# Kernel optimization log

Hardware: AMD Instinct MI355X
Metric: run time of the kernel (lower is better)

## Reference

```python
import jax, jax.numpy as jnp
import numpy as np

N_NODES = 50000
N_EDGES = 600000
N_GRAPHS = 256
IN_C = 128
HID = 128
OUT_C = 2


def setup_inputs() -> dict:
    key = jax.random.key(0)
    ks = jax.random.split(key, 16)
    d = {}
    d["x"] = jax.random.normal(ks[0], (N_NODES, IN_C), jnp.float32)
    d["edge_index"] = jax.random.randint(ks[1], (2, N_EDGES), 0, N_NODES, dtype=jnp.int32)
    d["root_node_idx"] = jax.random.randint(ks[2], (N_GRAPHS,), 0, N_NODES, dtype=jnp.int32)
    d["batch"] = jnp.sort(jax.random.randint(ks[3], (N_NODES,), 0, N_GRAPHS, dtype=jnp.int32))
    dims = [(IN_C, HID), (HID, HID), (HID, HID), (HID, HID)]
    for i, (ci, co) in enumerate(dims, start=1):
        s = 1.0 / np.sqrt(ci)
        d[f"w{i}_l"] = jax.random.uniform(ks[3 + i], (co, ci), jnp.float32, -s, s)
        d[f"b{i}_l"] = jnp.zeros((co,), jnp.float32)
        d[f"w{i}_r"] = jax.random.uniform(ks[7 + i], (co, ci), jnp.float32, -s, s)
    s = 1.0 / np.sqrt(2 * HID)
    d["w_cls"] = jax.random.uniform(ks[12], (OUT_C, 2 * HID), jnp.float32, -s, s)
    d["b_cls"] = jnp.zeros((OUT_C,), jnp.float32)
    return d


def _sage_conv(x, src, tgt, deg_inv, w_l, b_l, w_r):
    # mean aggregation of source features at target nodes (PyG SAGEConv, aggr='mean')
    agg = jax.ops.segment_sum(x[src], tgt, num_segments=N_NODES) * deg_inv  # [N, C]
    # out = lin_l(agg) + lin_r(x); lin_r has no bias in PyG SAGEConv
    return agg @ w_l.T + b_l + x @ w_r.T


def reference(x, edge_index, root_node_idx, batch,
              w1_l, b1_l, w1_r, w2_l, b2_l, w2_r,
              w3_l, b3_l, w3_r, w4_l, b4_l, w4_r,
              w_cls, b_cls):
    src, tgt = edge_index[0], edge_index[1]
    ones_e = jnp.ones((src.shape[0],), x.dtype)
    deg = jax.ops.segment_sum(ones_e, tgt, num_segments=N_NODES)
    deg_inv = (1.0 / jnp.maximum(deg, 1.0))[:, None]  # [N, 1]

    h = jax.nn.relu(_sage_conv(x, src, tgt, deg_inv, w1_l, b1_l, w1_r))
    h = jax.nn.relu(_sage_conv(h, src, tgt, deg_inv, w2_l, b2_l, w2_r))
    h = jax.nn.relu(_sage_conv(h, src, tgt, deg_inv, w3_l, b3_l, w3_r))
    h = jax.nn.relu(_sage_conv(h, src, tgt, deg_inv, w4_l, b4_l, w4_r))

    root_emb = h[root_node_idx]  # [G, HID]
    g_sum = jax.ops.segment_sum(h, batch, num_segments=N_GRAPHS)
    g_cnt = jax.ops.segment_sum(jnp.ones((h.shape[0],), h.dtype), batch, num_segments=N_GRAPHS)
    graph_emb = g_sum / jnp.maximum(g_cnt, 1.0)[:, None]  # [G, HID]

    combined = jnp.concatenate([root_emb, graph_emb], axis=1)  # [G, 2*HID]
    return combined @ w_cls.T + b_cls  # [G, OUT_C]
```

## Files before the change

### kernel.cpp

```cpp
#include <hip/hip_runtime.h>
#include <hip/hip_bf16.h>

#define N_NODES 50000
#define N_EDGES 600000
#define N_GRAPHS 256
#define C 128
#define NB 196

typedef unsigned short ushort;
typedef unsigned int uint;
typedef __attribute__((ext_vector_type(8))) short bfrag8;
typedef __attribute__((ext_vector_type(4))) float facc4;

__device__ __forceinline__ ushort f2bf(float v) {
    uint u = __float_as_uint(v);
    u += 0x7FFFu + ((u >> 16) & 1u);
    return (ushort)(u >> 16);
}
__device__ __forceinline__ float bf2f(ushort u) {
    return __uint_as_float(((uint)u) << 16);
}
__device__ __forceinline__ void fsplit(float v, ushort& h, ushort& l) {
    h = f2bf(v);
    l = f2bf(v - bf2f(h));
}

__global__ void k_deg(const int* __restrict__ tgt, int* __restrict__ deg) {
    int e = blockIdx.x * blockDim.x + threadIdx.x;
    if (e < N_EDGES) atomicAdd(&deg[tgt[e]], 1);
}

__global__ __launch_bounds__(256) void k_bsum(const int* __restrict__ deg,
                                              int* __restrict__ bsum,
                                              float* __restrict__ dinv) {
    __shared__ int ws[4];
    int idx = blockIdx.x * 256 + threadIdx.x;
    int v = (idx < N_NODES) ? deg[idx] : 0;
    if (idx < N_NODES) dinv[idx] = 1.0f / fmaxf((float)v, 1.0f);
    int s = v;
#pragma unroll
    for (int off = 1; off < 64; off <<= 1) s += __shfl_xor(s, off);
    if ((threadIdx.x & 63) == 0) ws[threadIdx.x >> 6] = s;
    __syncthreads();
    if (threadIdx.x == 0) bsum[blockIdx.x] = ws[0] + ws[1] + ws[2] + ws[3];
}

__global__ __launch_bounds__(256) void k_bscan(const int* __restrict__ bsum,
                                               int* __restrict__ boff,
                                               int* __restrict__ rowptr) {
    __shared__ int ws[4];
    int t = threadIdx.x, lane = t & 63, w = t >> 6;
    int v = (t < NB) ? bsum[t] : 0;
    int incl = v;
#pragma unroll
    for (int off = 1; off < 64; off <<= 1) {
        int u = __shfl_up(incl, off);
        if (lane >= off) incl += u;
    }
    if (lane == 63) ws[w] = incl;
    __syncthreads();
    int wo = 0;
    if (w > 0) wo += ws[0];
    if (w > 1) wo += ws[1];
    if (w > 2) wo += ws[2];
    if (t < NB) boff[t] = wo + incl - v;
    if (t == 0) rowptr[N_NODES] = N_EDGES;
}

__global__ __launch_bounds__(256) void k_rowptr(const int* __restrict__ deg,
                                                const int* __restrict__ boff,
                                                int* __restrict__ rowptr) {
    __shared__ int ws[4];
    int b = blockIdx.x, t = threadIdx.x;
    int idx = b * 256 + t;
    int lane = t & 63, w = t >> 6;
    int v = (idx < N_NODES) ? deg[idx] : 0;
    int incl = v;
#pragma unroll
    for (int off = 1; off < 64; off <<= 1) {
        int u = __shfl_up(incl, off);
        if (lane >= off) incl += u;
    }
    if (lane == 63) ws[w] = incl;
    __syncthreads();
    int wo = 0;
    if (w > 0) wo += ws[0];
    if (w > 1) wo += ws[1];
    if (w > 2) wo += ws[2];
    if (idx < N_NODES) rowptr[idx] = boff[b] + wo + incl - v;
}

__global__ void k_fill(const int* __restrict__ src, const int* __restrict__ tgt,
                       const int* __restrict__ rowptr, int* __restrict__ fill,
                       int* __restrict__ csr_src) {
    int e = blockIdx.x * blockDim.x + threadIdx.x;
    if (e >= N_EDGES) return;
    int d = tgt[e];
    int pos = atomicAdd(&fill[d], 1);
    csr_src[rowptr[d] + pos] = src[e];
}

__global__ __launch_bounds__(256) void k_xsplit(const float* __restrict__ x,
                                                ushort* __restrict__ Ahi,
                                                ushort* __restrict__ Alo) {
    int gid = blockIdx.x * 256 + threadIdx.x;
    if (gid >= N_NODES * 32) return;
    int n = gid >> 5, c4 = (gid & 31) << 2;
    float4 v = *(const float4*)(x + (size_t)n * C + c4);
    ushort4 h, l;
    fsplit(v.x, h.x, l.x); fsplit(v.y, h.y, l.y);
    fsplit(v.z, h.z, l.z); fsplit(v.w, h.w, l.w);
    *(ushort4*)(Ahi + (size_t)n * 256 + 128 + c4) = h;
    *(ushort4*)(Alo + (size_t)n * 256 + 128 + c4) = l;
}

struct WPtrs { const float* wl[4]; const float* wr[4]; };
__global__ __launch_bounds__(256) void k_wsplit(WPtrs wp, ushort* __restrict__ BTh,
                                                ushort* __restrict__ BTl) {
    int gid = blockIdx.x * 256 + threadIdx.x;
    if (gid >= 4 * 128 * 256) return;
    int l = gid >> 15;
    int rem = gid & 32767;
    int n = rem >> 8, k = rem & 255;
    float v = (k < 128) ? wp.wl[l][n * 128 + k] : wp.wr[l][n * 128 + (k - 128)];
    ushort h, lo;
    fsplit(v, h, lo);
    BTh[gid] = h;
    BTl[gid] = lo;
}

__global__ __launch_bounds__(256) void k_gather(const ushort* __restrict__ Ahi_r,
                                                const ushort* __restrict__ Alo_r,
                                                ushort* __restrict__ Ahi_w,
                                                ushort* __restrict__ Alo_w,
                                                const int* __restrict__ csr_src,
                                                const int* __restrict__ rowptr,
                                                const float* __restrict__ dinv) {
    int node = blockIdx.x * 16 + (threadIdx.x >> 4);
    if (node >= N_NODES) return;
    int c8 = (threadIdx.x & 15) << 3;
    int s = rowptr[node], e = rowptr[node + 1];
    float a[8] = {0.f, 0.f, 0.f, 0.f, 0.f, 0.f, 0.f, 0.f};
    int j = s;
    for (; j + 3 < e; j += 4) {
        int s0 = csr_src[j], s1 = csr_src[j + 1];
        int s2 = csr_src[j + 2], s3 = csr_src[j + 3];
        bfrag8 h0 = *(const bfrag8*)(Ahi_r + (size_t)s0 * 256 + 128 + c8);
        bfrag8 l0 = *(const bfrag8*)(Alo_r + (size_t)s0 * 256 + 128 + c8);
        bfrag8 h1 = *(const bfrag8*)(Ahi_r + (size_t)s1 * 256 + 128 + c8);
        bfrag8 l1 = *(const bfrag8*)(Alo_r + (size_t)s1 * 256 + 128 + c8);
        bfrag8 h2 = *(const bfrag8*)(Ahi_r + (size_t)s2 * 256 + 128 + c8);
        bfrag8 l2 = *(const bfrag8*)(Alo_r + (size_t)s2 * 256 + 128 + c8);
        bfrag8 h3 = *(const bfrag8*)(Ahi_r + (size_t)s3 * 256 + 128 + c8);
        bfrag8 l3 = *(const bfrag8*)(Alo_r + (size_t)s3 * 256 + 128 + c8);
#pragma unroll
        for (int c = 0; c < 8; c++)
            a[c] += (bf2f((ushort)h0[c]) + bf2f((ushort)l0[c]))
                  + (bf2f((ushort)h1[c]) + bf2f((ushort)l1[c]))
                  + (bf2f((ushort)h2[c]) + bf2f((ushort)l2[c]))
                  + (bf2f((ushort)h3[c]) + bf2f((ushort)l3[c]));
    }
    for (; j < e; j++) {
        int s0 = csr_src[j];
        bfrag8 h0 = *(const bfrag8*)(Ahi_r + (size_t)s0 * 256 + 128 + c8);
        bfrag8 l0 = *(const bfrag8*)(Alo_r + (size_t)s0 * 256 + 128 + c8);
#pragma unroll
        for (int c = 0; c < 8; c++)
            a[c] += bf2f((ushort)h0[c]) + bf2f((ushort)l0[c]);
    }
    float sc = dinv[node];
    bfrag8 oh, ol;
#pragma unroll
    for (int c = 0; c < 8; c++) {
        float v = a[c] * sc;
        ushort hh, ll;
        fsplit(v, hh, ll);
        oh[c] = (short)hh;
        ol[c] = (short)ll;
    }
    *(bfrag8*)(Ahi_w + (size_t)node * 256 + c8) = oh;
    *(bfrag8*)(Alo_w + (size_t)node * 256 + c8) = ol;
}

__global__ __launch_bounds__(256) void k_gemm(const ushort* __restrict__ Ahi,
                                              const ushort* __restrict__ Alo,
                                              const ushort* __restrict__ BTh,
                                              const ushort* __restrict__ BTl,
                                              const float* __restrict__ bl,
                                              ushort* __restrict__ Hhi,
                                              ushort* __restrict__ Hlo) {
    __shared__ __align__(16) short As[2][4096];
    const int tid = threadIdx.x;
    const int wave = tid >> 6, lane = tid & 63;
    const int m0 = blockIdx.x * 128;
    const int wm = (wave & 1) * 64;
    const int wn = (wave >> 1) * 64;
    const int l15 = lane & 15, lk = (lane >> 4) * 8;

    const ushort* sp[4];
    short* dp[4];
#pragma unroll
    for (int i = 0; i < 4; i++) {
        int gid = tid + i * 256;
        int p = gid >> 9, rem = gid & 511;
        int mt = rem >> 6, c = rem & 63;
        int row = m0 + mt * 16 + (c & 15);
        if (row >= N_NODES) row = N_NODES - 1;
        sp[i] = (p ? Alo : Ahi) + (size_t)row * 256 + ((c >> 4) << 3);
        dp[i] = &As[p][mt * 512 + c * 8];
    }
    const ushort* pBh[4];
    const ushort* pBl[4];
#pragma unroll
    for (int t = 0; t < 4; t++) {
        int n = wn + t * 16 + l15;
        pBh[t] = BTh + n * 256 + lk;
        pBl[t] = BTl + n * 256 + lk;
    }

    bfrag8 r[4];
#define LOADSTEP(K0) do { \
        r[0] = *(const bfrag8*)(sp[0] + (K0)); \
        r[1] = *(const bfrag8*)(sp[1] + (K0)); \
        r[2] = *(const bfrag8*)(sp[2] + (K0)); \
        r[3] = *(const bfrag8*)(sp[3] + (K0)); \
    } while (0)

    LOADSTEP(0);
    facc4 acc[4][4] = {};
#pragma unroll
    for (int s = 0; s < 8; s++) {
        *(bfrag8*)dp[0] = r[0];
        *(bfrag8*)dp[1] = r[1];
        *(bfrag8*)dp[2] = r[2];
        *(bfrag8*)dp[3] = r[3];
        __syncthreads();
        if (s < 7) LOADSTEP((s + 1) * 32);
        const int k0 = s * 32;
        bfrag8 b[2][4], a[2][4];
#pragma unroll
        for (int t = 0; t < 4; t++) {
            b[0][t] = *(const bfrag8*)(pBh[t] + k0);
            b[1][t] = *(const bfrag8*)(pBl[t] + k0);
        }
#pragma unroll
        for (int t = 0; t < 4; t++) {
            int mt = (wm >> 4) + t;
            a[0][t] = *(const bfrag8*)&As[0][mt * 512 + lane * 8];
            a[1][t] = *(const bfrag8*)&As[1][mt * 512 + lane * 8];
        }
#pragma unroll
        for (int mt = 0; mt < 4; mt++)
#pragma unroll
            for (int nt = 0; nt < 4; nt++) {
                acc[mt][nt] = __builtin_amdgcn_mfma_f32_16x16x32_bf16(a[0][mt], b[0][nt], acc[mt][nt], 0, 0, 0);
                acc[mt][nt] = __builtin_amdgcn_mfma_f32_16x16x32_bf16(a[0][mt], b[1][nt], acc[mt][nt], 0, 0, 0);
                acc[mt][nt] = __builtin_amdgcn_mfma_f32_16x16x32_bf16(a[1][mt], b[0][nt], acc[mt][nt], 0, 0, 0);
            }
        __syncthreads();
    }
#undef LOADSTEP

    const int r4 = (lane >> 4) * 4;
#pragma unroll
    for (int mt = 0; mt < 4; mt++) {
#pragma unroll
        for (int nt = 0; nt < 4; nt++) {
            int col = wn + nt * 16 + l15;
            float bias = bl[col];
#pragma unroll
            for (int rr = 0; rr < 4; rr++) {
                int grow = m0 + wm + mt * 16 + r4 + rr;
                if (grow < N_NODES) {
                    float v = fmaxf(acc[mt][nt][rr] + bias, 0.f);
                    ushort h, l;
                    fsplit(v, h, l);
                    Hhi[(size_t)grow * 256 + 128 + col] = h;
                    Hlo[(size_t)grow * 256 + 128 + col] = l;
                }
            }
        }
    }
}

__global__ void k_gstart(const int* __restrict__ batch, int* __restrict__ gstart) {
    int g = blockIdx.x * blockDim.x + threadIdx.x;
    if (g > N_GRAPHS) return;
    int lo = 0, hi = N_NODES;
    while (lo < hi) {
        int mid = (lo + hi) >> 1;
        if (batch[mid] < g) lo = mid + 1;
        else hi = mid;
    }
    gstart[g] = lo;
}

__global__ __launch_bounds__(512) void k_pool(const ushort* __restrict__ Ahi,
                                              const ushort* __restrict__ Alo,
                                              const int* __restrict__ gstart,
                                              float* __restrict__ gmean) {
    __shared__ float part[4][C];
    int g = blockIdx.x;
    int c = threadIdx.x & 127, p = threadIdx.x >> 7;
    int s = gstart[g], e = gstart[g + 1];
    float sum = 0.f;
    for (int n = s + p; n < e; n += 4) {
        size_t o = (size_t)n * 256 + 128 + c;
        sum += bf2f(Ahi[o]) + bf2f(Alo[o]);
    }
    part[p][c] = sum;
    __syncthreads();
    if (p == 0) {
        float tot = part[0][c] + part[1][c] + part[2][c] + part[3][c];
        float cnt = fmaxf((float)(e - s), 1.0f);
        gmean[g * C + c] = tot / cnt;
    }
}

__global__ __launch_bounds__(256) void k_final(const ushort* __restrict__ Ahi,
                                               const ushort* __restrict__ Alo,
                                               const float* __restrict__ gmean,
                                               const int* __restrict__ root,
                                               const float* __restrict__ wcls,
                                               const float* __restrict__ bcls,
                                               float* __restrict__ out) {
    __shared__ float red[8];
    int g = blockIdx.x, t = threadIdx.x;
    float v;
    if (t < 128) {
        size_t o = (size_t)root[g] * 256 + 128 + t;
        v = bf2f(Ahi[o]) + bf2f(Alo[o]);
    } else {
        v = gmean[g * C + (t - 128)];
    }
    float p0 = v * wcls[t];
    float p1 = v * wcls[256 + t];
#pragma unroll
    for (int off = 32; off; off >>= 1) {
        p0 += __shfl_down(p0, off);
        p1 += __shfl_down(p1, off);
    }
    int wid = t >> 6;
    if ((t & 63) == 0) { red[wid] = p0; red[4 + wid] = p1; }
    __syncthreads();
    if (t == 0) {
        out[g * 2 + 0] = red[0] + red[1] + red[2] + red[3] + bcls[0];
        out[g * 2 + 1] = red[4] + red[5] + red[6] + red[7] + bcls[1];
    }
}

extern "C" void kernel_launch(void* const* d_in, const int* in_sizes, int n_in,
                              void* d_out, int out_size, void* d_ws, size_t ws_size,
                              hipStream_t stream) {
    const float* x = (const float*)d_in[0];
    const int* ei = (const int*)d_in[1];
    const int* src = ei;
    const int* tgt = ei + N_EDGES;
    const int* root = (const int*)d_in[2];
    const int* batch = (const int*)d_in[3];
    WPtrs wp;
    wp.wl[0] = (const float*)d_in[4];  wp.wr[0] = (const float*)d_in[6];
    wp.wl[1] = (const float*)d_in[7];  wp.wr[1] = (const float*)d_in[9];
    wp.wl[2] = (const float*)d_in[10]; wp.wr[2] = (const float*)d_in[12];
    wp.wl[3] = (const float*)d_in[13]; wp.wr[3] = (const float*)d_in[15];
    const float* blv[4] = {(const float*)d_in[5], (const float*)d_in[8],
                           (const float*)d_in[11], (const float*)d_in[14]};
    const float* wcls = (const float*)d_in[16];
    const float* bcls = (const float*)d_in[17];
    float* out = (float*)d_out;

    ushort* Ahi = (ushort*)d_ws;
    ushort* Alo = Ahi + (size_t)N_NODES * 256;
    ushort* BTh = Alo + (size_t)N_NODES * 256;
    ushort* BTl = BTh + 4 * 128 * 256;
    int* deg = (int*)(BTl + 4 * 128 * 256);
    float* dinv = (float*)(deg + N_NODES);
    int* rowptr = (int*)(dinv + N_NODES);
    int* fill = rowptr + N_NODES + 1;
    int* csr_src = fill + N_NODES;
    int* bsum = csr_src + N_EDGES;
    int* boff = bsum + 256;
    int* gstart = boff + 256;
    float* gmean = (float*)(gstart + 260);

    hipMemsetAsync(deg, 0, N_NODES * sizeof(int), stream);
    hipMemsetAsync(fill, 0, N_NODES * sizeof(int), stream);
    k_deg<<<(N_EDGES + 255) / 256, 256, 0, stream>>>(tgt, deg);
    k_bsum<<<NB, 256, 0, stream>>>(deg, bsum, dinv);
    k_bscan<<<1, 256, 0, stream>>>(bsum, boff, rowptr);
    k_rowptr<<<NB, 256, 0, stream>>>(deg, boff, rowptr);
    k_fill<<<(N_EDGES + 255) / 256, 256, 0, stream>>>(src, tgt, rowptr, fill, csr_src);
    k_gstart<<<1, 512, 0, stream>>>(batch, gstart);
    k_xsplit<<<(N_NODES * 32 + 255) / 256, 256, 0, stream>>>(x, Ahi, Alo);
    k_wsplit<<<(4 * 128 * 256 + 255) / 256, 256, 0, stream>>>(wp, BTh, BTl);

    for (int l = 0; l < 4; l++) {
        k_gather<<<(N_NODES + 15) / 16, 256, 0, stream>>>(Ahi, Alo, Ahi, Alo,
                                                          csr_src, rowptr, dinv);
        k_gemm<<<(N_NODES + 127) / 128, 256, 0, stream>>>(
            Ahi, Alo, BTh + l * 32768, BTl + l * 32768, blv[l], Ahi, Alo);
    }
    k_pool<<<N_GRAPHS, 512, 0, stream>>>(Ahi, Alo, gstart, gmean);
    k_final<<<N_GRAPHS, 256, 0, stream>>>(Ahi, Alo, gmean, root, wcls, bcls, out);
}
```

Before: 523.7 us.

## Shrink GEMM M-tile to 64, preload full A tile, stage epilogue through LDS

The GEMM block tile drops from 128 to 64 rows, which doubles the grid to about 782 blocks. Each of the four waves now owns a 64x32 output slice. The whole A tile (hi and lo, all of K) is loaded into 64KB of shared memory once, replacing the per-K-step double load and its sync pairs. The epilogue writes accumulators to LDS, then each thread handles 32 contiguous columns of one row and emits vectorized 16-byte bf16 hi/lo stores instead of scattered 2-byte stores. The cost is larger LDS use per block, which limits occupancy, and no overlap between the A load and the MFMA work.

```diff
diff --git a/kernel.cpp b/kernel.cpp
--- a/kernel.cpp
+++ b/kernel.cpp
@@ -189,96 +189,112 @@
                                               const float* __restrict__ bl,
                                               ushort* __restrict__ Hhi,
                                               ushort* __restrict__ Hlo) {
-    __shared__ __align__(16) short As[2][4096];
+    __shared__ __align__(16) short As[32768];
     const int tid = threadIdx.x;
     const int wave = tid >> 6, lane = tid & 63;
-    const int m0 = blockIdx.x * 128;
-    const int wm = (wave & 1) * 64;
-    const int wn = (wave >> 1) * 64;
+    const int m0 = blockIdx.x * 64;
+    const int wn = wave * 32;
     const int l15 = lane & 15, lk = (lane >> 4) * 8;
 
-    const ushort* sp[4];
-    short* dp[4];
-#pragma unroll
-    for (int i = 0; i < 4; i++) {
-        int gid = tid + i * 256;
-        int p = gid >> 9, rem = gid & 511;
-        int mt = rem >> 6, c = rem & 63;
-        int row = m0 + mt * 16 + (c & 15);
-        if (row >= N_NODES) row = N_NODES - 1;
-        sp[i] = (p ? Alo : Ahi) + (size_t)row * 256 + ((c >> 4) << 3);
-        dp[i] = &As[p][mt * 512 + c * 8];
-    }
-    const ushort* pBh[4];
-    const ushort* pBl[4];
-#pragma unroll
-    for (int t = 0; t < 4; t++) {
+#pragma unroll
+    for (int half = 0; half < 2; half++) {
+        bfrag8 r[8];
+#pragma unroll
+        for (int i = 0; i < 8; i++) {
+            int gid = (half * 8 + i) * 256 + tid;
+            int p = gid >> 11;
+            int rem = gid & 2047;
+            int mt = rem >> 9;
+            int cc = rem & 511;
+            int s = cc >> 6, l = cc & 63;
+            int row = m0 + mt * 16 + (l & 15);
+            if (row >= N_NODES) row = N_NODES - 1;
+            const ushort* base = p ? Alo : Ahi;
+            r[i] = *(const bfrag8*)(base + (size_t)row * 256 + s * 32 + (l >> 4) * 8);
+        }
+#pragma unroll
+        for (int i = 0; i < 8; i++) {
+            int gid = (half * 8 + i) * 256 + tid;
+            *(bfrag8*)&As[gid * 8] = r[i];
+        }
+    }
+    __syncthreads();
+
+    const ushort* pBh[2];
+    const ushort* pBl[2];
+#pragma unroll
+    for (int t = 0; t < 2; t++) {
         int n = wn + t * 16 + l15;
         pBh[t] = BTh + n * 256 + lk;
         pBl[t] = BTl + n * 256 + lk;
     }
 
-    bfrag8 r[4];
-#define LOADSTEP(K0) do { \
-        r[0] = *(const bfrag8*)(sp[0] + (K0)); \
-        r[1] = *(const bfrag8*)(sp[1] + (K0)); \
-        r[2] = *(const bfrag8*)(sp[2] + (K0)); \
-        r[3] = *(const bfrag8*)(sp[3] + (K0)); \
-    } while (0)
-
-    LOADSTEP(0);
-    facc4 acc[4][4] = {};
+    facc4 acc[4][2] = {};
 #pragma unroll
     for (int s = 0; s < 8; s++) {
-        *(bfrag8*)dp[0] = r[0];
-        *(bfrag8*)dp[1] = r[1];
-        *(bfrag8*)dp[2] = r[2];
-        *(bfrag8*)dp[3] = r[3];
-        __syncthreads();
-        if (s < 7) LOADSTEP((s + 1) * 32);
-        const int k0 = s * 32;
-        bfrag8 b[2][4], a[2][4];
-#pragma unroll
-        for (int t = 0; t < 4; t++) {
-            b[0][t] = *(const bfrag8*)(pBh[t] + k0);
-            b[1][t] = *(const bfrag8*)(pBl[t] + k0);
-        }
-#pragma unroll
-        for (int t = 0; t < 4; t++) {
-            int mt = (wm >> 4) + t;
-            a[0][t] = *(const bfrag8*)&As[0][mt * 512 + lane * 8];
-            a[1][t] = *(const bfrag8*)&As[1][mt * 512 + lane * 8];
+        bfrag8 bh[2], blv[2];
+#pragma unroll
+        for (int t = 0; t < 2; t++) {
+            bh[t]  = *(const bfrag8*)(pBh[t] + s * 32);
+            blv[t] = *(const bfrag8*)(pBl[t] + s * 32);
+        }
+        bfrag8 a0[4], a1[4];
+#pragma unroll
+        for (int mt = 0; mt < 4; mt++) {
+            a0[mt] = *(const bfrag8*)&As[(mt * 512 + s * 64 + lane) * 8];
+            a1[mt] = *(const bfrag8*)&As[(2048 + mt * 512 + s * 64 + lane) * 8];
         }
 #pragma unroll
         for (int mt = 0; mt < 4; mt++)
 #pragma unroll
-            for (int nt = 0; nt < 4; nt++) {
-                acc[mt][nt] = __builtin_amdgcn_mfma_f32_16x16x32_bf16(a[0][mt], b[0][nt], acc[mt][nt], 0, 0, 0);
-                acc[mt][nt] = __builtin_amdgcn_mfma_f32_16x16x32_bf16(a[0][mt], b[1][nt], acc[mt][nt], 0, 0, 0);
-                acc[mt][nt] = __builtin_amdgcn_mfma_f32_16x16x32_bf16(a[1][mt], b[0][nt], acc[mt][nt], 0, 0, 0);
+            for (int nt = 0; nt < 2; nt++) {
+                acc[mt][nt] = __builtin_amdgcn_mfma_f32_16x16x32_bf16(a0[mt], bh[nt],  acc[mt][nt], 0, 0, 0);
+                acc[mt][nt] = __builtin_amdgcn_mfma_f32_16x16x32_bf16(a0[mt], blv[nt], acc[mt][nt], 0, 0, 0);
+                acc[mt][nt] = __builtin_amdgcn_mfma_f32_16x16x32_bf16(a1[mt], bh[nt],  acc[mt][nt], 0, 0, 0);
             }
-        __syncthreads();
-    }
-#undef LOADSTEP
-
+    }
+    __syncthreads();
+
+    float* smf = (float*)As;
     const int r4 = (lane >> 4) * 4;
 #pragma unroll
-    for (int mt = 0; mt < 4; mt++) {
-#pragma unroll
-        for (int nt = 0; nt < 4; nt++) {
-            int col = wn + nt * 16 + l15;
-            float bias = bl[col];
+    for (int mt = 0; mt < 4; mt++)
+#pragma unroll
+        for (int nt = 0; nt < 2; nt++) {
+            int cl = wn + nt * 16 + l15;
 #pragma unroll
             for (int rr = 0; rr < 4; rr++) {
-                int grow = m0 + wm + mt * 16 + r4 + rr;
-                if (grow < N_NODES) {
-                    float v = fmaxf(acc[mt][nt][rr] + bias, 0.f);
-                    ushort h, l;
-                    fsplit(v, h, l);
-                    Hhi[(size_t)grow * 256 + 128 + col] = h;
-                    Hlo[(size_t)grow * 256 + 128 + col] = l;
-                }
+                int rl = mt * 16 + r4 + rr;
+                smf[rl * 132 + cl] = acc[mt][nt][rr];
             }
+        }
+    __syncthreads();
+    const int erow = tid >> 2;
+    const int ecs = (tid & 3) * 32;
+    int grow = m0 + erow;
+    if (grow < N_NODES) {
+        float vals[32];
+#pragma unroll
+        for (int q = 0; q < 8; q++) {
+            float4 sv = *(const float4*)&smf[erow * 132 + ecs + q * 4];
+            float4 bv = *(const float4*)(bl + ecs + q * 4);
+            vals[q * 4 + 0] = fmaxf(sv.x + bv.x, 0.f);
+            vals[q * 4 + 1] = fmaxf(sv.y + bv.y, 0.f);
+            vals[q * 4 + 2] = fmaxf(sv.z + bv.z, 0.f);
+            vals[q * 4 + 3] = fmaxf(sv.w + bv.w, 0.f);
+        }
+#pragma unroll
+        for (int q = 0; q < 4; q++) {
+            bfrag8 ho, lo;
+#pragma unroll
+            for (int c = 0; c < 8; c++) {
+                ushort hh, ll;
+                fsplit(vals[q * 8 + c], hh, ll);
+                ho[c] = (short)hh;
+                lo[c] = (short)ll;
+            }
+            *(bfrag8*)(Hhi + (size_t)grow * 256 + 128 + ecs + q * 8) = ho;
+            *(bfrag8*)(Hlo + (size_t)grow * 256 + 128 + ecs + q * 8) = lo;
         }
     }
 }
@@ -397,7 +413,7 @@
     for (int l = 0; l < 4; l++) {
         k_gather<<<(N_NODES + 15) / 16, 256, 0, stream>>>(Ahi, Alo, Ahi, Alo,
                                                           csr_src, rowptr, dinv);
-        k_gemm<<<(N_NODES + 127) / 128, 256, 0, stream>>>(
+        k_gemm<<<(N_NODES + 63) / 64, 256, 0, stream>>>(
             Ahi, Alo, BTh + l * 32768, BTl + l * 32768, blv[l], Ahi, Alo);
     }
     k_pool<<<N_GRAPHS, 512, 0, stream>>>(Ahi, Alo, gstart, gmean);
```

After: 527.3 us. No clear change (+0.7%).
